# Optimization experiments

Measured on AMD Instinct MI355X. Metric: run time of the kernel, lower is better.

The kernel has to match this reference:

```python
import jax, jax.numpy as jnp
import numpy as np
import math

M = 512          # num_bin_x
NB = 512         # num_bin_y
NUM_NODES = 2_000_000
K = 4            # max bins a node can overlap per dim (size <= 2.5 bins)
SQRT2 = math.sqrt(2.0)


def setup_inputs() -> dict:
    key = jax.random.key(0)
    k1, k2 = jax.random.split(key)
    node_pos = jax.random.uniform(k1, (NUM_NODES, 2), jnp.float32, 0.05, 0.95)
    # node sizes between 0.5 and 2.5 bins (normalized layout units)
    node_size = jax.random.uniform(k2, (NUM_NODES, 2), jnp.float32) * (2.0 / M) + (0.5 / M)
    return {
        "node_pos": node_pos,
        "node_size": node_size,
        "node_weight": jnp.ones((NUM_NODES,), jnp.float32),
        "expand_ratio": jnp.ones((NUM_NODES,), jnp.float32),
        "unit_len": jnp.array([1.0 / M, 1.0 / NB], jnp.float32),
        "init_density_map": jnp.zeros((M, NB), jnp.float32),
        "num_bin_x": M,
        "num_bin_y": NB,
    }


def pre_normalize(node_pos, node_size, node_weight, expand_ratio, unit_len, mx, ny):
    # density_map_cuda.pre_normalize: expand tiny nodes to sqrt(2)*unit_len,
    # rescale weight to preserve area, convert rects to bin coordinates.
    ux, uy = unit_len[0], unit_len[1]
    w, h = node_size[:, 0], node_size[:, 1]
    new_w = jnp.maximum(w, SQRT2 * ux)
    new_h = jnp.maximum(h, SQRT2 * uy)
    weight = node_weight * expand_ratio * (w * h) / (new_w * new_h)
    xl = jnp.clip((node_pos[:, 0] - 0.5 * new_w) / ux, 0.0, mx)
    xh = jnp.clip((node_pos[:, 0] + 0.5 * new_w) / ux, 0.0, mx)
    yl = jnp.clip((node_pos[:, 1] - 0.5 * new_h) / uy, 0.0, ny)
    yh = jnp.clip((node_pos[:, 1] + 0.5 * new_h) / uy, 0.0, ny)
    return jnp.stack([xl, xh, yl, yh, weight], axis=1)  # [N, 5]


def scatter_density(info, mx, ny):
    # density_map_cuda.forward: overlap-area scatter-add of node rects into bins.
    xl, xh, yl, yh, w = info[:, 0], info[:, 1], info[:, 2], info[:, 3], info[:, 4]
    bx0 = jnp.floor(xl).astype(jnp.int32)
    by0 = jnp.floor(yl).astype(jnp.int32)
    dm = jnp.zeros((mx, ny), jnp.float32)
    for dx in range(K):
        ix = bx0 + dx
        fx = ix.astype(jnp.float32)
        ox = jnp.clip(jnp.minimum(xh, fx + 1.0) - jnp.maximum(xl, fx), 0.0)
        ixc = jnp.clip(ix, 0, mx - 1)
        for dy in range(K):
            iy = by0 + dy
            fy = iy.astype(jnp.float32)
            oy = jnp.clip(jnp.minimum(yh, fy + 1.0) - jnp.maximum(yl, fy), 0.0)
            iyc = jnp.clip(iy, 0, ny - 1)
            dm = dm.at[ixc, iyc].add(w * ox * oy)
    return dm


def make_transforms(n):
    k = jnp.arange(n, dtype=jnp.float32)[:, None]
    m = jnp.arange(n, dtype=jnp.float32)[None, :]
    ang = jnp.pi * k * (2.0 * m + 1.0) / (2.0 * n)
    C = jnp.cos(ang)  # [freq, space]
    S = jnp.sin(ang)
    w = jnp.where(jnp.arange(n) == 0, 1.0, 2.0).astype(jnp.float32)
    return C, S, w


def spectral_solve(dm, unit_len, mx, ny):
    # fft_scale construction from __init__
    wj = (jnp.arange(mx, dtype=jnp.float32) * (2.0 * jnp.pi / mx))[:, None]
    wk = (jnp.arange(ny, dtype=jnp.float32) * (2.0 * jnp.pi / ny))[None, :]
    wk = wk * (unit_len[0] / unit_len[1])  # scale_w_k=True
    wsq = wj ** 2 + wk ** 2
    wsq = wsq.at[0, 0].set(1.0)
    pscale = (1.0 / wsq).at[0, 0].set(0.0)
    fx_scale = wj * pscale * 0.5
    fy_scale = wk * pscale * 0.5

    Cx, Sx, wx = make_transforms(mx)
    Cy, Sy, wy = make_transforms(ny)
    # dct2: coeff[u,v] = (1/(M*N)) * sum_{m,n} dm[m,n] cos(pi u(2m+1)/2M) cos(pi v(2n+1)/2N)
    coeff = (Cx @ dm @ Cy.T) / (mx * ny)
    ICx = (wx[:, None] * Cx)  # weighted inverse cosine basis [freq, space]
    ICy = (wy[:, None] * Cy)
    ISx = (wx[:, None] * Sx)
    ISy = (wy[:, None] * Sy)
    potential = ICx.T @ (coeff * pscale) @ ICy          # idct2
    force_x = ISx.T @ (coeff * fx_scale) @ ICy          # idxst_idct
    force_y = ICx.T @ (coeff * fy_scale) @ ISy          # idct_idxst
    return potential, force_x, force_y


def reference(node_pos, node_size, node_weight, expand_ratio, unit_len,
              init_density_map, num_bin_x, num_bin_y):
    info = pre_normalize(node_pos, node_size, node_weight, expand_ratio,
                         unit_len, num_bin_x, num_bin_y)
    density_map = init_density_map + scatter_density(info, num_bin_x, num_bin_y)
    potential, _, _ = spectral_solve(density_map, unit_len, num_bin_x, num_bin_y)
    energy = jnp.sum(potential * density_map)
    return energy
```

## Files before the change

### kernel.cpp

```cpp
#include <hip/hip_runtime.h>
#include <math.h>

#define MX 512
#define NY 512
#define TWO_PI 6.283185307179586f

#define TILE_SHIFT 4
#define TILES_SIDE 32
#define NTILES 1024
#define NPB 8192
#define LOCAL_DIM 20
#define SLAB_ELEMS (LOCAL_DIM * LOCAL_DIM)
#define CAP 4096

typedef __attribute__((ext_vector_type(8))) short short8;
typedef __attribute__((ext_vector_type(4))) float float4_t;

__device__ __forceinline__ unsigned short f2bf(float x) {
    union { float f; unsigned u; } v; v.f = x;
    unsigned r = v.u + 0x7fffu + ((v.u >> 16) & 1u);
    return (unsigned short)(r >> 16);
}
__device__ __forceinline__ float bf2f(unsigned short h) {
    union { float f; unsigned u; } v; v.u = ((unsigned)h) << 16;
    return v.f;
}

__device__ __forceinline__ void node_bounds(float2 p, float2 s, float ux, float uy,
                                            float& xl, float& xh, float& yl, float& yh,
                                            float& nw, float& nh) {
    const float SQ2 = 1.41421356237309515f;
    nw = fmaxf(s.x, SQ2 * ux);
    nh = fmaxf(s.y, SQ2 * uy);
    xl = fminf(fmaxf((p.x - 0.5f * nw) / ux, 0.0f), (float)MX);
    xh = fminf(fmaxf((p.x + 0.5f * nw) / ux, 0.0f), (float)MX);
    yl = fminf(fmaxf((p.y - 0.5f * nh) / uy, 0.0f), (float)NY);
    yh = fminf(fmaxf((p.y + 0.5f * nh) / uy, 0.0f), (float)NY);
}

__global__ void init_cap_kernel(unsigned int* __restrict__ base,
                                unsigned int* __restrict__ cursor) {
    int t = blockIdx.x * blockDim.x + threadIdx.x;
    if (t <= NTILES) {
        base[t] = (unsigned int)t * CAP;
        if (t < NTILES) cursor[t] = (unsigned int)t * CAP;
    }
}

__global__ __launch_bounds__(256)
void count_kernel(const float2* __restrict__ pos, const float2* __restrict__ size,
                  const float* __restrict__ unit_len,
                  unsigned int* __restrict__ cnt, int n) {
    __shared__ unsigned int h[NTILES];
    for (int t = threadIdx.x; t < NTILES; t += 256) h[t] = 0;
    __syncthreads();
    float ux = unit_len[0], uy = unit_len[1];
    int start = blockIdx.x * NPB;
    int end = min(start + NPB, n);
    for (int i = start + (int)threadIdx.x; i < end; i += 256) {
        float xl, xh, yl, yh, nw, nh;
        node_bounds(pos[i], size[i], ux, uy, xl, xh, yl, yh, nw, nh);
        int bx0 = min((int)floorf(xl), MX - 1);
        int by0 = min((int)floorf(yl), NY - 1);
        int t = ((bx0 >> TILE_SHIFT) << 5) | (by0 >> TILE_SHIFT);
        atomicAdd(&h[t], 1u);
    }
    __syncthreads();
    for (int t = threadIdx.x; t < NTILES; t += 256) {
        unsigned int c = h[t];
        if (c) atomicAdd(&cnt[t], c);
    }
}

__global__ __launch_bounds__(256)
void scan_kernel(const unsigned int* __restrict__ cnt,
                 unsigned int* __restrict__ base,
                 unsigned int* __restrict__ cursor) {
    __shared__ unsigned int s[256];
    int tid = threadIdx.x;
    unsigned int loc[4];
    unsigned int sum = 0;
#pragma unroll
    for (int k = 0; k < 4; k++) { loc[k] = cnt[tid * 4 + k]; sum += loc[k]; }
    s[tid] = sum;
    __syncthreads();
    for (int off = 1; off < 256; off <<= 1) {
        unsigned int v = (tid >= off) ? s[tid - off] : 0u;
        __syncthreads();
        s[tid] += v;
        __syncthreads();
    }
    unsigned int ex = (tid == 0) ? 0u : s[tid - 1];
#pragma unroll
    for (int k = 0; k < 4; k++) {
        base[tid * 4 + k] = ex;
        cursor[tid * 4 + k] = ex;
        ex += loc[k];
    }
    if (tid == 255) base[NTILES] = ex;
}

__global__ __launch_bounds__(256)
void place_payload_kernel(const float2* __restrict__ pos, const float2* __restrict__ size,
                          const float* __restrict__ nwt, const float* __restrict__ er,
                          const float* __restrict__ unit_len,
                          const unsigned int* __restrict__ base,
                          unsigned int* __restrict__ cursor,
                          float4* __restrict__ pb, float* __restrict__ pw, int n) {
    __shared__ unsigned int h[NTILES];
    __shared__ unsigned int bb[NTILES];
    for (int t = threadIdx.x; t < NTILES; t += 256) h[t] = 0;
    __syncthreads();
    float ux = unit_len[0], uy = unit_len[1];
    int start = blockIdx.x * NPB;
    int end = min(start + NPB, n);
    unsigned int packed[NPB / 256];
#pragma unroll
    for (int k = 0; k < NPB / 256; k++) {
        int i = start + k * 256 + (int)threadIdx.x;
        if (i < end) {
            float xl, xh, yl, yh, nw, nh;
            node_bounds(pos[i], size[i], ux, uy, xl, xh, yl, yh, nw, nh);
            int bx0 = min((int)floorf(xl), MX - 1);
            int by0 = min((int)floorf(yl), NY - 1);
            unsigned int t = ((bx0 >> TILE_SHIFT) << 5) | (by0 >> TILE_SHIFT);
            packed[k] = (t << 13) | atomicAdd(&h[t], 1u);
        }
    }
    __syncthreads();
    for (int t = threadIdx.x; t < NTILES; t += 256) {
        unsigned int c = h[t];
        if (c) bb[t] = atomicAdd(&cursor[t], c);
    }
    __syncthreads();
#pragma unroll
    for (int k = 0; k < NPB / 256; k++) {
        int i = start + k * 256 + (int)threadIdx.x;
        if (i < end) {
            float2 p = pos[i], s = size[i];
            float xl, xh, yl, yh, nw, nh;
            node_bounds(p, s, ux, uy, xl, xh, yl, yh, nw, nh);
            float w = nwt[i] * er[i] * (s.x * s.y) / (nw * nh);
            unsigned int t = packed[k] >> 13;
            unsigned int dst = bb[t] + (packed[k] & 8191u);
            if (dst < base[t + 1]) {
                pb[dst] = make_float4(xl, xh, yl, yh);
                pw[dst] = w;
            }
        }
    }
}

__global__ __launch_bounds__(256)
void accum_slab_kernel(const float4* __restrict__ pb, const float* __restrict__ pw,
                       const unsigned int* __restrict__ base,
                       const unsigned int* __restrict__ cursor,
                       float* __restrict__ slab) {
    __shared__ float acc[LOCAL_DIM][LOCAL_DIM + 1];
    int t = blockIdx.x >> 1;
    int half = blockIdx.x & 1;
    int tbx = (t >> 5) << TILE_SHIFT;
    int tby = (t & 31) << TILE_SHIFT;
    for (int e = threadIdx.x; e < SLAB_ELEMS; e += 256)
        acc[e / LOCAL_DIM][e % LOCAL_DIM] = 0.0f;
    __syncthreads();

    unsigned int b0 = base[t];
    unsigned int c = min(cursor[t] - b0, base[t + 1] - b0);
    unsigned int chunk = (c + 1) >> 1;
    unsigned int ks = half * chunk;
    unsigned int ke = min(c, ks + chunk);
    for (unsigned int k = ks + threadIdx.x; k < ke; k += 256) {
        float4 b4 = pb[b0 + k];
        float w = pw[b0 + k];
        float xl = b4.x, xh = b4.y, yl = b4.z, yh = b4.w;
        int bx0 = min((int)floorf(xl), MX - 1);
        int by0 = min((int)floorf(yl), NY - 1);
        float oxs[4], oys[4];
        int lxs[4], lys[4];
#pragma unroll
        for (int d = 0; d < 4; d++) {
            int ix = bx0 + d;
            float fx = (float)ix;
            oxs[d] = fmaxf(fminf(xh, fx + 1.0f) - fmaxf(xl, fx), 0.0f);
            lxs[d] = min(max(min(ix, MX - 1) - tbx, 0), LOCAL_DIM - 1);
            int iy = by0 + d;
            float fy = (float)iy;
            oys[d] = fmaxf(fminf(yh, fy + 1.0f) - fmaxf(yl, fy), 0.0f);
            lys[d] = min(max(min(iy, NY - 1) - tby, 0), LOCAL_DIM - 1);
        }
#pragma unroll
        for (int dx = 0; dx < 4; dx++) {
            if (oxs[dx] == 0.0f) continue;
            float wox = w * oxs[dx];
#pragma unroll
            for (int dy = 0; dy < 4; dy++) {
                float v = wox * oys[dy];
                if (v != 0.0f) atomicAdd(&acc[lxs[dx]][lys[dy]], v);
            }
        }
    }
    __syncthreads();
    float* dst = slab + (size_t)blockIdx.x * SLAB_ELEMS;
    for (int e = threadIdx.x; e < SLAB_ELEMS; e += 256)
        dst[e] = acc[e / LOCAL_DIM][e % LOCAL_DIM];
}

__global__ __launch_bounds__(256)
void combine_kernel(const float* __restrict__ slab,
                    const float* __restrict__ init_dm,
                    unsigned short* __restrict__ dmh,
                    unsigned short* __restrict__ dml) {
    int idx = blockIdx.x * blockDim.x + threadIdx.x;
    int gx = idx >> 9, gy = idx & 511;
    float sum = init_dm[idx];
    int tx0 = gx >> 4, ty0 = gy >> 4;
    int rx = gx & 15, ry = gy & 15;
#pragma unroll
    for (int ax = 0; ax < 2; ax++) {
        int tx = tx0 - ax;
        if (tx < 0 || (ax == 1 && rx > 3)) continue;
        int lx = rx + ax * 16;
#pragma unroll
        for (int ay = 0; ay < 2; ay++) {
            int ty = ty0 - ay;
            if (ty < 0 || (ay == 1 && ry > 3)) continue;
            int ly = ry + ay * 16;
            const float* s0 = slab + ((size_t)((tx << 5) | ty) * 2) * SLAB_ELEMS
                                   + lx * LOCAL_DIM + ly;
            sum += s0[0] + s0[SLAB_ELEMS];
        }
    }
    unsigned short hi = f2bf(sum);
    dmh[idx] = hi;
    dml[idx] = f2bf(sum - bf2f(hi));
}

__global__ __launch_bounds__(256)
void scatter_kernel(const float2* __restrict__ pos, const float2* __restrict__ size,
                    const float* __restrict__ nwt, const float* __restrict__ er,
                    const float* __restrict__ unit_len,
                    float* __restrict__ dm, int n) {
    int i = blockIdx.x * blockDim.x + threadIdx.x;
    if (i >= n) return;
    float ux = unit_len[0], uy = unit_len[1];
    float2 p = pos[i], s = size[i];
    float xl, xh, yl, yh, nw, nh;
    node_bounds(p, s, ux, uy, xl, xh, yl, yh, nw, nh);
    float w = nwt[i] * er[i] * (s.x * s.y) / (nw * nh);
    int bx0 = (int)floorf(xl);
    int by0 = (int)floorf(yl);
#pragma unroll
    for (int dx = 0; dx < 4; dx++) {
        int ix = bx0 + dx;
        float fx = (float)ix;
        float ox = fmaxf(fminf(xh, fx + 1.0f) - fmaxf(xl, fx), 0.0f);
        if (ox == 0.0f) continue;
        int rowoff = min(max(ix, 0), MX - 1) * NY;
        float wox = w * ox;
#pragma unroll
        for (int dy = 0; dy < 4; dy++) {
            int iy = by0 + dy;
            float fy = (float)iy;
            float oy = fmaxf(fminf(yh, fy + 1.0f) - fmaxf(yl, fy), 0.0f);
            float v = wox * oy;
            if (v != 0.0f) atomicAdd(&dm[rowoff + min(max(iy, 0), NY - 1)], v);
        }
    }
}

__global__ void cvt_dm_kernel(const float* __restrict__ dm,
                              unsigned short* __restrict__ dmh,
                              unsigned short* __restrict__ dml) {
    int idx = blockIdx.x * blockDim.x + threadIdx.x;
    float x = dm[idx];
    unsigned short hi = f2bf(x);
    dmh[idx] = hi;
    dml[idx] = f2bf(x - bf2f(hi));
}

__global__ void gen_cos_kernel(unsigned short* __restrict__ Ch,
                               unsigned short* __restrict__ Cl) {
    int idx = blockIdx.x * blockDim.x + threadIdx.x;
    int a = idx >> 9;
    int j = idx & 511;
    float x = cospif((float)(a * (2 * j + 1)) * (1.0f / 1024.0f));
    unsigned short hi = f2bf(x);
    Ch[idx] = hi;
    Cl[idx] = f2bf(x - bf2f(hi));
}

__global__ __launch_bounds__(256)
void dct1_mfma_kernel(const unsigned short* __restrict__ dmh,
                      const unsigned short* __restrict__ dml,
                      const unsigned short* __restrict__ Ch,
                      const unsigned short* __restrict__ Cl,
                      unsigned short* __restrict__ UhT,
                      unsigned short* __restrict__ UlT) {
    int lane = threadIdx.x & 63;
    int wv = threadIdx.x >> 6;
    int tile = blockIdx.x * 4 + wv;
    int jt = (tile >> 5) * 16;
    int bt = (tile & 31) * 16;
    int m = lane & 15, q = lane >> 4;
    float4_t acc = {0.f, 0.f, 0.f, 0.f};
    const unsigned short* ah_row = dmh + (jt + m) * 512;
    const unsigned short* al_row = dml + (jt + m) * 512;
    const unsigned short* bh_row = Ch + (bt + m) * 512;
    const unsigned short* bl_row = Cl + (bt + m) * 512;
#pragma unroll 4
    for (int k0 = 0; k0 < 512; k0 += 32) {
        int off = k0 + q * 8;
        short8 ah = *(const short8*)(ah_row + off);
        short8 al = *(const short8*)(al_row + off);
        short8 bh = *(const short8*)(bh_row + off);
        short8 bl = *(const short8*)(bl_row + off);
        acc = __builtin_amdgcn_mfma_f32_16x16x32_bf16(ah, bh, acc, 0, 0, 0);
        acc = __builtin_amdgcn_mfma_f32_16x16x32_bf16(ah, bl, acc, 0, 0, 0);
        acc = __builtin_amdgcn_mfma_f32_16x16x32_bf16(al, bh, acc, 0, 0, 0);
    }
#pragma unroll
    for (int r = 0; r < 4; r++) {
        float v = acc[r];
        unsigned short hi = f2bf(v);
        int addr = (bt + m) * 512 + jt + q * 4 + r;
        UhT[addr] = hi;
        UlT[addr] = f2bf(v - bf2f(hi));
    }
}

__global__ __launch_bounds__(256)
void dct2_mfma_kernel(const unsigned short* __restrict__ Ch,
                      const unsigned short* __restrict__ Cl,
                      const unsigned short* __restrict__ UhT,
                      const unsigned short* __restrict__ UlT,
                      const float* __restrict__ unit_len,
                      float* __restrict__ out) {
    __shared__ float red[4];
    int lane = threadIdx.x & 63;
    int wv = threadIdx.x >> 6;
    int tile = blockIdx.x * 4 + wv;
    int at = (tile >> 5) * 16;
    int bt = (tile & 31) * 16;
    int m = lane & 15, q = lane >> 4;
    float4_t acc = {0.f, 0.f, 0.f, 0.f};
    const unsigned short* ah_row = Ch + (at + m) * 512;
    const unsigned short* al_row = Cl + (at + m) * 512;
    const unsigned short* bh_row = UhT + (bt + m) * 512;
    const unsigned short* bl_row = UlT + (bt + m) * 512;
#pragma unroll 4
    for (int k0 = 0; k0 < 512; k0 += 32) {
        int off = k0 + q * 8;
        short8 ah = *(const short8*)(ah_row + off);
        short8 al = *(const short8*)(al_row + off);
        short8 bh = *(const short8*)(bh_row + off);
        short8 bl = *(const short8*)(bl_row + off);
        acc = __builtin_amdgcn_mfma_f32_16x16x32_bf16(ah, bh, acc, 0, 0, 0);
        acc = __builtin_amdgcn_mfma_f32_16x16x32_bf16(ah, bl, acc, 0, 0, 0);
        acc = __builtin_amdgcn_mfma_f32_16x16x32_bf16(al, bh, acc, 0, 0, 0);
    }
    float ratio = unit_len[0] / unit_len[1];
    int b = bt + m;
    float wkb = (float)b * (TWO_PI / (float)NY) * ratio;
    float wyb = (b == 0) ? 1.0f : 2.0f;
    float e = 0.0f;
#pragma unroll
    for (int r = 0; r < 4; r++) {
        int a = at + q * 4 + r;
        float wja = (float)a * (TWO_PI / (float)MX);
        float wsq = wja * wja + wkb * wkb;
        float ps = (a == 0 && b == 0) ? 0.0f : (1.0f / wsq);
        float wxa = (a == 0) ? 1.0f : 2.0f;
        e += wxa * wyb * ps * acc[r] * acc[r];
    }
#pragma unroll
    for (int off = 32; off > 0; off >>= 1) e += __shfl_down(e, off, 64);
    if (lane == 0) red[wv] = e;
    __syncthreads();
    if (threadIdx.x == 0) {
        float t = red[0] + red[1] + red[2] + red[3];
        atomicAdd(out, t * (1.0f / ((float)MX * (float)NY)));
    }
}

extern "C" void kernel_launch(void* const* d_in, const int* in_sizes, int n_in,
                              void* d_out, int out_size, void* d_ws, size_t ws_size,
                              hipStream_t stream) {
    const float2* node_pos  = (const float2*)d_in[0];
    const float2* node_size = (const float2*)d_in[1];
    const float*  node_wt   = (const float*)d_in[2];
    const float*  exp_ratio = (const float*)d_in[3];
    const float*  unit_len  = (const float*)d_in[4];
    const float*  init_dm   = (const float*)d_in[5];
    float* out = (float*)d_out;
    int n = in_sizes[2];

    char* wsb = (char*)d_ws;
    size_t off = 0;
    auto alloc = [&](size_t bytes) { void* p = wsb + off; off = (off + bytes + 255) & ~(size_t)255; return p; };
    unsigned short* Ch   = (unsigned short*)alloc((size_t)MX * NY * 2);
    unsigned short* Cl   = (unsigned short*)alloc((size_t)MX * NY * 2);
    unsigned short* dmh  = (unsigned short*)alloc((size_t)MX * NY * 2);
    unsigned short* dml  = (unsigned short*)alloc((size_t)MX * NY * 2);
    unsigned short* UhT  = (unsigned short*)alloc((size_t)MX * NY * 2);
    unsigned short* UlT  = (unsigned short*)alloc((size_t)MX * NY * 2);
    float*          dm     = (float*)alloc((size_t)MX * NY * sizeof(float));
    unsigned int*   cnt    = (unsigned int*)alloc(NTILES * sizeof(unsigned int));
    unsigned int*   tbase  = (unsigned int*)alloc((NTILES + 1) * sizeof(unsigned int));
    unsigned int*   cursor = (unsigned int*)alloc(NTILES * sizeof(unsigned int));
    float*          slab   = (float*)alloc((size_t)NTILES * 2 * SLAB_ELEMS * sizeof(float));
    size_t off_common = off;
    float4* pbF = (float4*)alloc((size_t)NTILES * CAP * sizeof(float4));
    float*  pwF = (float*)alloc((size_t)NTILES * CAP * sizeof(float));
    bool tierFast = (off <= ws_size);
    off = off_common;
    float4* pbE = (float4*)alloc((size_t)n * sizeof(float4));
    float*  pwE = (float*)alloc((size_t)n * sizeof(float));
    bool tierExact = (off <= ws_size);

    hipMemsetAsync(d_out, 0, sizeof(float), stream);
    gen_cos_kernel<<<(MX * NY) / 256, 256, 0, stream>>>(Ch, Cl);

    if (tierFast || tierExact) {
        float4* pb = tierFast ? pbF : pbE;
        float*  pw = tierFast ? pwF : pwE;
        int nblk = (n + NPB - 1) / NPB;
        if (tierFast) {
            init_cap_kernel<<<5, 256, 0, stream>>>(tbase, cursor);
        } else {
            hipMemsetAsync(cnt, 0, NTILES * sizeof(unsigned int), stream);
            count_kernel<<<nblk, 256, 0, stream>>>(node_pos, node_size, unit_len, cnt, n);
            scan_kernel<<<1, 256, 0, stream>>>(cnt, tbase, cursor);
        }
        place_payload_kernel<<<nblk, 256, 0, stream>>>(
            node_pos, node_size, node_wt, exp_ratio, unit_len, tbase, cursor,
            pb, pw, n);
        accum_slab_kernel<<<NTILES * 2, 256, 0, stream>>>(pb, pw, tbase, cursor, slab);
        combine_kernel<<<(MX * NY) / 256, 256, 0, stream>>>(slab, init_dm, dmh, dml);
    } else {
        hipMemcpyAsync(dm, init_dm, (size_t)MX * NY * sizeof(float),
                       hipMemcpyDeviceToDevice, stream);
        scatter_kernel<<<(n + 255) / 256, 256, 0, stream>>>(
            node_pos, node_size, node_wt, exp_ratio, unit_len, dm, n);
        cvt_dm_kernel<<<(MX * NY) / 256, 256, 0, stream>>>(dm, dmh, dml);
    }

    dct1_mfma_kernel<<<NTILES / 4, 256, 0, stream>>>(dmh, dml, Ch, Cl, UhT, UlT);
    dct2_mfma_kernel<<<NTILES / 4, 256, 0, stream>>>(Ch, Cl, UhT, UlT, unit_len, out);
}
```

Measured before the change: 287.2 us.

## Switch density scatter to 64x64 tiles with adaptive split accumulation

Replaces 1024 small 16x16 bin tiles and a fixed-capacity bucket tier with 64 large tiles, always using an exact count/scan/place counting sort, and splits each tile across a workspace-dependent number of accumulation blocks. Place now caches node bounds and weights in registers instead of recomputing. This aims to cut per-tile overhead and halo waste, at the cost of an extra counting pass over inputs, more partial slabs to sum in combine, and more shared-atomic contention per tile.

New measurement: 297.7 us. 1.04x slower.

```diff
diff --git a/kernel.cpp b/kernel.cpp
--- a/kernel.cpp
+++ b/kernel.cpp
@@ -5,13 +5,13 @@
 #define NY 512
 #define TWO_PI 6.283185307179586f
 
-#define TILE_SHIFT 4
-#define TILES_SIDE 32
-#define NTILES 1024
-#define NPB 8192
-#define LOCAL_DIM 20
-#define SLAB_ELEMS (LOCAL_DIM * LOCAL_DIM)
-#define CAP 4096
+#define TSHIFT 6
+#define TSIDE 8
+#define NT 64
+#define LDIM 68
+#define SLAB (LDIM * LDIM)
+#define NPB 2048
+#define KPT 8
 
 typedef __attribute__((ext_vector_type(8))) short short8;
 typedef __attribute__((ext_vector_type(4))) float float4_t;
@@ -38,137 +38,118 @@
     yh = fminf(fmaxf((p.y + 0.5f * nh) / uy, 0.0f), (float)NY);
 }
 
-__global__ void init_cap_kernel(unsigned int* __restrict__ base,
-                                unsigned int* __restrict__ cursor) {
-    int t = blockIdx.x * blockDim.x + threadIdx.x;
-    if (t <= NTILES) {
-        base[t] = (unsigned int)t * CAP;
-        if (t < NTILES) cursor[t] = (unsigned int)t * CAP;
-    }
-}
-
 __global__ __launch_bounds__(256)
 void count_kernel(const float2* __restrict__ pos, const float2* __restrict__ size,
                   const float* __restrict__ unit_len,
                   unsigned int* __restrict__ cnt, int n) {
-    __shared__ unsigned int h[NTILES];
-    for (int t = threadIdx.x; t < NTILES; t += 256) h[t] = 0;
+    __shared__ unsigned int h[NT];
+    if (threadIdx.x < NT) h[threadIdx.x] = 0;
     __syncthreads();
     float ux = unit_len[0], uy = unit_len[1];
     int start = blockIdx.x * NPB;
     int end = min(start + NPB, n);
-    for (int i = start + (int)threadIdx.x; i < end; i += 256) {
-        float xl, xh, yl, yh, nw, nh;
-        node_bounds(pos[i], size[i], ux, uy, xl, xh, yl, yh, nw, nh);
-        int bx0 = min((int)floorf(xl), MX - 1);
-        int by0 = min((int)floorf(yl), NY - 1);
-        int t = ((bx0 >> TILE_SHIFT) << 5) | (by0 >> TILE_SHIFT);
-        atomicAdd(&h[t], 1u);
-    }
-    __syncthreads();
-    for (int t = threadIdx.x; t < NTILES; t += 256) {
-        unsigned int c = h[t];
-        if (c) atomicAdd(&cnt[t], c);
-    }
-}
-
-__global__ __launch_bounds__(256)
-void scan_kernel(const unsigned int* __restrict__ cnt,
-                 unsigned int* __restrict__ base,
-                 unsigned int* __restrict__ cursor) {
-    __shared__ unsigned int s[256];
-    int tid = threadIdx.x;
-    unsigned int loc[4];
-    unsigned int sum = 0;
-#pragma unroll
-    for (int k = 0; k < 4; k++) { loc[k] = cnt[tid * 4 + k]; sum += loc[k]; }
-    s[tid] = sum;
-    __syncthreads();
-    for (int off = 1; off < 256; off <<= 1) {
-        unsigned int v = (tid >= off) ? s[tid - off] : 0u;
-        __syncthreads();
-        s[tid] += v;
-        __syncthreads();
-    }
-    unsigned int ex = (tid == 0) ? 0u : s[tid - 1];
-#pragma unroll
-    for (int k = 0; k < 4; k++) {
-        base[tid * 4 + k] = ex;
-        cursor[tid * 4 + k] = ex;
-        ex += loc[k];
-    }
-    if (tid == 255) base[NTILES] = ex;
-}
-
-__global__ __launch_bounds__(256)
-void place_payload_kernel(const float2* __restrict__ pos, const float2* __restrict__ size,
-                          const float* __restrict__ nwt, const float* __restrict__ er,
-                          const float* __restrict__ unit_len,
-                          const unsigned int* __restrict__ base,
-                          unsigned int* __restrict__ cursor,
-                          float4* __restrict__ pb, float* __restrict__ pw, int n) {
-    __shared__ unsigned int h[NTILES];
-    __shared__ unsigned int bb[NTILES];
-    for (int t = threadIdx.x; t < NTILES; t += 256) h[t] = 0;
-    __syncthreads();
-    float ux = unit_len[0], uy = unit_len[1];
-    int start = blockIdx.x * NPB;
-    int end = min(start + NPB, n);
-    unsigned int packed[NPB / 256];
-#pragma unroll
-    for (int k = 0; k < NPB / 256; k++) {
+#pragma unroll
+    for (int k = 0; k < KPT; k++) {
         int i = start + k * 256 + (int)threadIdx.x;
         if (i < end) {
             float xl, xh, yl, yh, nw, nh;
             node_bounds(pos[i], size[i], ux, uy, xl, xh, yl, yh, nw, nh);
             int bx0 = min((int)floorf(xl), MX - 1);
             int by0 = min((int)floorf(yl), NY - 1);
-            unsigned int t = ((bx0 >> TILE_SHIFT) << 5) | (by0 >> TILE_SHIFT);
-            packed[k] = (t << 13) | atomicAdd(&h[t], 1u);
-        }
-    }
-    __syncthreads();
-    for (int t = threadIdx.x; t < NTILES; t += 256) {
-        unsigned int c = h[t];
-        if (c) bb[t] = atomicAdd(&cursor[t], c);
-    }
-    __syncthreads();
-#pragma unroll
-    for (int k = 0; k < NPB / 256; k++) {
+            int t = ((bx0 >> TSHIFT) << 3) | (by0 >> TSHIFT);
+            atomicAdd(&h[t], 1u);
+        }
+    }
+    __syncthreads();
+    if (threadIdx.x < NT) {
+        unsigned int c = h[threadIdx.x];
+        if (c) atomicAdd(&cnt[threadIdx.x], c);
+    }
+}
+
+__global__ void scan_kernel(const unsigned int* __restrict__ cnt,
+                            unsigned int* __restrict__ base,
+                            unsigned int* __restrict__ cursor) {
+    if (threadIdx.x == 0 && blockIdx.x == 0) {
+        unsigned int ex = 0;
+        for (int t = 0; t < NT; t++) {
+            base[t] = ex;
+            cursor[t] = ex;
+            ex += cnt[t];
+        }
+        base[NT] = ex;
+    }
+}
+
+__global__ __launch_bounds__(256)
+void place_kernel(const float2* __restrict__ pos, const float2* __restrict__ size,
+                  const float* __restrict__ nwt, const float* __restrict__ er,
+                  const float* __restrict__ unit_len,
+                  const unsigned int* __restrict__ base,
+                  unsigned int* __restrict__ cursor,
+                  float4* __restrict__ pb, float* __restrict__ pw, int n) {
+    __shared__ unsigned int h[NT];
+    __shared__ unsigned int bb[NT];
+    if (threadIdx.x < NT) h[threadIdx.x] = 0;
+    __syncthreads();
+    float ux = unit_len[0], uy = unit_len[1];
+    int start = blockIdx.x * NPB;
+    int end = min(start + NPB, n);
+
+    float cxl[KPT], cxh[KPT], cyl[KPT], cyh[KPT], cw[KPT];
+    unsigned int pk[KPT];
+#pragma unroll
+    for (int k = 0; k < KPT; k++) {
         int i = start + k * 256 + (int)threadIdx.x;
         if (i < end) {
             float2 p = pos[i], s = size[i];
             float xl, xh, yl, yh, nw, nh;
             node_bounds(p, s, ux, uy, xl, xh, yl, yh, nw, nh);
-            float w = nwt[i] * er[i] * (s.x * s.y) / (nw * nh);
-            unsigned int t = packed[k] >> 13;
-            unsigned int dst = bb[t] + (packed[k] & 8191u);
+            cxl[k] = xl; cxh[k] = xh; cyl[k] = yl; cyh[k] = yh;
+            cw[k] = nwt[i] * er[i] * (s.x * s.y) / (nw * nh);
+            int bx0 = min((int)floorf(xl), MX - 1);
+            int by0 = min((int)floorf(yl), NY - 1);
+            unsigned int t = ((bx0 >> TSHIFT) << 3) | (by0 >> TSHIFT);
+            pk[k] = (t << 11) | atomicAdd(&h[t], 1u);
+        }
+    }
+    __syncthreads();
+    if (threadIdx.x < NT) {
+        unsigned int c = h[threadIdx.x];
+        bb[threadIdx.x] = c ? atomicAdd(&cursor[threadIdx.x], c) : 0u;
+    }
+    __syncthreads();
+#pragma unroll
+    for (int k = 0; k < KPT; k++) {
+        int i = start + k * 256 + (int)threadIdx.x;
+        if (i < end) {
+            unsigned int t = pk[k] >> 11;
+            unsigned int dst = bb[t] + (pk[k] & 2047u);
             if (dst < base[t + 1]) {
-                pb[dst] = make_float4(xl, xh, yl, yh);
-                pw[dst] = w;
+                pb[dst] = make_float4(cxl[k], cxh[k], cyl[k], cyh[k]);
+                pw[dst] = cw[k];
             }
         }
     }
 }
 
 __global__ __launch_bounds__(256)
-void accum_slab_kernel(const float4* __restrict__ pb, const float* __restrict__ pw,
-                       const unsigned int* __restrict__ base,
-                       const unsigned int* __restrict__ cursor,
-                       float* __restrict__ slab) {
-    __shared__ float acc[LOCAL_DIM][LOCAL_DIM + 1];
-    int t = blockIdx.x >> 1;
-    int half = blockIdx.x & 1;
-    int tbx = (t >> 5) << TILE_SHIFT;
-    int tby = (t & 31) << TILE_SHIFT;
-    for (int e = threadIdx.x; e < SLAB_ELEMS; e += 256)
-        acc[e / LOCAL_DIM][e % LOCAL_DIM] = 0.0f;
+void accum_kernel(const float4* __restrict__ pb, const float* __restrict__ pw,
+                  const unsigned int* __restrict__ base,
+                  float* __restrict__ slab, int spt) {
+    __shared__ float acc[LDIM][LDIM + 1];
+    int t = blockIdx.x / spt;
+    int s = blockIdx.x - t * spt;
+    int tbx = (t >> 3) << TSHIFT;
+    int tby = (t & 7) << TSHIFT;
+    for (int e = threadIdx.x; e < SLAB; e += 256)
+        acc[e / LDIM][e % LDIM] = 0.0f;
     __syncthreads();
 
     unsigned int b0 = base[t];
-    unsigned int c = min(cursor[t] - b0, base[t + 1] - b0);
-    unsigned int chunk = (c + 1) >> 1;
-    unsigned int ks = half * chunk;
+    unsigned int c = base[t + 1] - b0;
+    unsigned int chunk = (c + spt - 1) / spt;
+    unsigned int ks = s * chunk;
     unsigned int ke = min(c, ks + chunk);
     for (unsigned int k = ks + threadIdx.x; k < ke; k += 256) {
         float4 b4 = pb[b0 + k];
@@ -183,11 +164,11 @@
             int ix = bx0 + d;
             float fx = (float)ix;
             oxs[d] = fmaxf(fminf(xh, fx + 1.0f) - fmaxf(xl, fx), 0.0f);
-            lxs[d] = min(max(min(ix, MX - 1) - tbx, 0), LOCAL_DIM - 1);
+            lxs[d] = min(max(min(ix, MX - 1) - tbx, 0), LDIM - 1);
             int iy = by0 + d;
             float fy = (float)iy;
             oys[d] = fmaxf(fminf(yh, fy + 1.0f) - fmaxf(yl, fy), 0.0f);
-            lys[d] = min(max(min(iy, NY - 1) - tby, 0), LOCAL_DIM - 1);
+            lys[d] = min(max(min(iy, NY - 1) - tby, 0), LDIM - 1);
         }
 #pragma unroll
         for (int dx = 0; dx < 4; dx++) {
@@ -201,34 +182,34 @@
         }
     }
     __syncthreads();
-    float* dst = slab + (size_t)blockIdx.x * SLAB_ELEMS;
-    for (int e = threadIdx.x; e < SLAB_ELEMS; e += 256)
-        dst[e] = acc[e / LOCAL_DIM][e % LOCAL_DIM];
+    float* dst = slab + (size_t)blockIdx.x * SLAB;
+    for (int e = threadIdx.x; e < SLAB; e += 256)
+        dst[e] = acc[e / LDIM][e % LDIM];
 }
 
 __global__ __launch_bounds__(256)
 void combine_kernel(const float* __restrict__ slab,
                     const float* __restrict__ init_dm,
                     unsigned short* __restrict__ dmh,
-                    unsigned short* __restrict__ dml) {
+                    unsigned short* __restrict__ dml, int spt) {
     int idx = blockIdx.x * blockDim.x + threadIdx.x;
     int gx = idx >> 9, gy = idx & 511;
     float sum = init_dm[idx];
-    int tx0 = gx >> 4, ty0 = gy >> 4;
-    int rx = gx & 15, ry = gy & 15;
+    int tx0 = gx >> TSHIFT, ty0 = gy >> TSHIFT;
+    int rx = gx & 63, ry = gy & 63;
 #pragma unroll
     for (int ax = 0; ax < 2; ax++) {
         int tx = tx0 - ax;
         if (tx < 0 || (ax == 1 && rx > 3)) continue;
-        int lx = rx + ax * 16;
+        int lx = rx + (ax << TSHIFT);
 #pragma unroll
         for (int ay = 0; ay < 2; ay++) {
             int ty = ty0 - ay;
             if (ty < 0 || (ay == 1 && ry > 3)) continue;
-            int ly = ry + ay * 16;
-            const float* s0 = slab + ((size_t)((tx << 5) | ty) * 2) * SLAB_ELEMS
-                                   + lx * LOCAL_DIM + ly;
-            sum += s0[0] + s0[SLAB_ELEMS];
+            int ly = ry + (ay << TSHIFT);
+            const float* s0 = slab + (size_t)(((tx << 3) | ty) * spt) * SLAB
+                                   + lx * LDIM + ly;
+            for (int s = 0; s < spt; s++) sum += s0[(size_t)s * SLAB];
         }
     }
     unsigned short hi = f2bf(sum);
@@ -405,38 +386,36 @@
     unsigned short* UhT  = (unsigned short*)alloc((size_t)MX * NY * 2);
     unsigned short* UlT  = (unsigned short*)alloc((size_t)MX * NY * 2);
     float*          dm     = (float*)alloc((size_t)MX * NY * sizeof(float));
-    unsigned int*   cnt    = (unsigned int*)alloc(NTILES * sizeof(unsigned int));
-    unsigned int*   tbase  = (unsigned int*)alloc((NTILES + 1) * sizeof(unsigned int));
-    unsigned int*   cursor = (unsigned int*)alloc(NTILES * sizeof(unsigned int));
-    float*          slab   = (float*)alloc((size_t)NTILES * 2 * SLAB_ELEMS * sizeof(float));
-    size_t off_common = off;
-    float4* pbF = (float4*)alloc((size_t)NTILES * CAP * sizeof(float4));
-    float*  pwF = (float*)alloc((size_t)NTILES * CAP * sizeof(float));
-    bool tierFast = (off <= ws_size);
-    off = off_common;
-    float4* pbE = (float4*)alloc((size_t)n * sizeof(float4));
-    float*  pwE = (float*)alloc((size_t)n * sizeof(float));
-    bool tierExact = (off <= ws_size);
+    unsigned int*   cnt    = (unsigned int*)alloc(NT * sizeof(unsigned int));
+    unsigned int*   tbase  = (unsigned int*)alloc((NT + 1) * sizeof(unsigned int));
+    unsigned int*   cursor = (unsigned int*)alloc(NT * sizeof(unsigned int));
+    float4*         pb     = (float4*)alloc((size_t)n * sizeof(float4));
+    float*          pw     = (float*)alloc((size_t)n * sizeof(float));
+    bool binned = (off <= ws_size);
+    int spt = 0;
+    float* slab = nullptr;
+    if (binned) {
+        size_t avail = ws_size - off;
+        size_t per_spt = (size_t)NT * SLAB * sizeof(float);
+        spt = (int)(avail / per_spt);
+        if (spt > 32) spt = 32;
+        if (spt < 1) binned = false;
+        else slab = (float*)alloc((size_t)NT * spt * SLAB * sizeof(float));
+    }
 
     hipMemsetAsync(d_out, 0, sizeof(float), stream);
     gen_cos_kernel<<<(MX * NY) / 256, 256, 0, stream>>>(Ch, Cl);
 
-    if (tierFast || tierExact) {
-        float4* pb = tierFast ? pbF : pbE;
-        float*  pw = tierFast ? pwF : pwE;
+    if (binned) {
+        hipMemsetAsync(cnt, 0, NT * sizeof(unsigned int), stream);
         int nblk = (n + NPB - 1) / NPB;
-        if (tierFast) {
-            init_cap_kernel<<<5, 256, 0, stream>>>(tbase, cursor);
-        } else {
-            hipMemsetAsync(cnt, 0, NTILES * sizeof(unsigned int), stream);
-            count_kernel<<<nblk, 256, 0, stream>>>(node_pos, node_size, unit_len, cnt, n);
-            scan_kernel<<<1, 256, 0, stream>>>(cnt, tbase, cursor);
-        }
-        place_payload_kernel<<<nblk, 256, 0, stream>>>(
+        count_kernel<<<nblk, 256, 0, stream>>>(node_pos, node_size, unit_len, cnt, n);
+        scan_kernel<<<1, 64, 0, stream>>>(cnt, tbase, cursor);
+        place_kernel<<<nblk, 256, 0, stream>>>(
             node_pos, node_size, node_wt, exp_ratio, unit_len, tbase, cursor,
             pb, pw, n);
-        accum_slab_kernel<<<NTILES * 2, 256, 0, stream>>>(pb, pw, tbase, cursor, slab);
-        combine_kernel<<<(MX * NY) / 256, 256, 0, stream>>>(slab, init_dm, dmh, dml);
+        accum_kernel<<<NT * spt, 256, 0, stream>>>(pb, pw, tbase, slab, spt);
+        combine_kernel<<<(MX * NY) / 256, 256, 0, stream>>>(slab, init_dm, dmh, dml, spt);
     } else {
         hipMemcpyAsync(dm, init_dm, (size_t)MX * NY * sizeof(float),
                        hipMemcpyDeviceToDevice, stream);
@@ -445,6 +424,6 @@
         cvt_dm_kernel<<<(MX * NY) / 256, 256, 0, stream>>>(dm, dmh, dml);
     }
 
-    dct1_mfma_kernel<<<NTILES / 4, 256, 0, stream>>>(dmh, dml, Ch, Cl, UhT, UlT);
-    dct2_mfma_kernel<<<NTILES / 4, 256, 0, stream>>>(Ch, Cl, UhT, UlT, unit_len, out);
-}
+    dct1_mfma_kernel<<<256, 256, 0, stream>>>(dmh, dml, Ch, Cl, UhT, UlT);
+    dct2_mfma_kernel<<<256, 256, 0, stream>>>(Ch, Cl, UhT, UlT, unit_len, out);
+}
```
